# Kernel optimization log

Measured on AMD Instinct MI355X. Metric: run time of the kernel, lower is better.

## Reference

```python
import jax, jax.numpy as jnp
import numpy as np

T, N, L = 512, 128, 256           # encoder steps, batch, decode steps
KV, VS = 128, 128                 # key_size, value_size
EMB, HID, VOC = 256, 512, 34


def _lstm_cell(x, h, c, W_ih, W_hh, b_ih, b_hh):
    # PyTorch LSTMCell gate order: i, f, g, o
    g = x @ W_ih.T + b_ih + h @ W_hh.T + b_hh
    i, f, gg, o = jnp.split(g, 4, axis=-1)
    c2 = jax.nn.sigmoid(f) * c + jax.nn.sigmoid(i) * jnp.tanh(gg)
    h2 = jax.nn.sigmoid(o) * jnp.tanh(c2)
    return h2, c2


def setup_inputs() -> dict:
    k = jax.random.key(0)
    ks = jax.random.split(k, 16)
    s = 0.05
    return {
        "key": jax.random.normal(ks[0], (T, N, KV), jnp.float32),
        "values": jax.random.normal(ks[1], (T, N, VS), jnp.float32),
        "lens": jax.random.randint(ks[2], (N,), 1, T + 1),
        "text": jax.random.randint(ks[3], (N, L), 0, VOC),
        "emb": jax.random.normal(ks[4], (VOC, EMB), jnp.float32) * s,
        "W_ih1": jax.random.normal(ks[5], (4 * HID, EMB + VS), jnp.float32) * s,
        "W_hh1": jax.random.normal(ks[6], (4 * HID, HID), jnp.float32) * s,
        "b_ih1": jnp.zeros((4 * HID,), jnp.float32),
        "b_hh1": jnp.zeros((4 * HID,), jnp.float32),
        "W_ih2": jax.random.normal(ks[7], (4 * KV, HID), jnp.float32) * s,
        "W_hh2": jax.random.normal(ks[8], (4 * KV, KV), jnp.float32) * s,
        "b_ih2": jnp.zeros((4 * KV,), jnp.float32),
        "b_hh2": jnp.zeros((4 * KV,), jnp.float32),
        "W_out": jax.random.normal(ks[9], (VOC, KV + VS), jnp.float32) * s,
        "b_out": jnp.zeros((VOC,), jnp.float32),
    }


def reference(key, values, lens, text, emb, W_ih1, W_hh1, b_ih1, b_hh1,
              W_ih2, W_hh2, b_ih2, b_hh2, W_out, b_out):
    # key/values: (T, N, 128); teacher-forced decode over L steps.
    pad_mask = jnp.arange(T)[None, :] >= lens[:, None]        # (N, T)
    embs = emb[text]                                          # (N, L, EMB)
    embs = jnp.transpose(embs, (1, 0, 2))                     # (L, N, EMB)

    def step(carry, e_t):
        h1, c1, h2, c2, ctx = carry
        x = jnp.concatenate([e_t, ctx], axis=-1)
        h1, c1 = _lstm_cell(x, h1, c1, W_ih1, W_hh1, b_ih1, b_hh1)
        h2, c2 = _lstm_cell(h1, h2, c2, W_ih2, W_hh2, b_ih2, b_hh2)
        # masked bmm attention: energy (N, T)
        energy = jnp.einsum('tnk,nk->nt', key, h2)
        energy = jnp.where(pad_mask, -1e9, energy)
        attn = jax.nn.softmax(energy, axis=1)
        ctx = jnp.einsum('nt,tnv->nv', attn, values)
        pred = jnp.concatenate([h2, ctx], axis=-1) @ W_out.T + b_out
        return (h1, c1, h2, c2, ctx), pred

    init = (jnp.zeros((N, HID)), jnp.zeros((N, HID)),
            jnp.zeros((N, KV)), jnp.zeros((N, KV)),
            jnp.zeros((N, VS)))
    _, preds = jax.lax.scan(step, init, embs)                 # (L, N, VOC)
    return jnp.transpose(preds, (1, 0, 2))                    # (N, L, VOC)
```

## Files before the change

kernel.cpp:

```cpp
#include <hip/hip_runtime.h>
#include <hip/hip_cooperative_groups.h>
#include <math.h>

#define LDEC 256
#define VOCD 34
#define SPIN_MAX 2000000u
#define XSTR 660

typedef __attribute__((ext_vector_type(8))) short bf16x8;
typedef __attribute__((ext_vector_type(8))) unsigned short u16x8;
typedef __attribute__((ext_vector_type(4))) float f32x4;

#define OFF_W1H  0u
#define OFF_W1L  2621440u
#define OFF_W2H  5242880u
#define OFF_W2L  5898240u
#define OFF_EG   6553600u
#define OFF_B2   6832128u
#define OFF_WOT  6834176u
#define OFF_H1P  6868992u
#define OFF_H2P  7393280u
#define OFF_CTXP 7524352u
#define OFF_C1   7589888u
#define OFF_C2   7852032u
#define OFF_FLG  7917568u
#define OFF_KB   7966720u
#define OFF_VB   24743936u
#define WS_NEED  41521152u

__device__ __forceinline__ float sigf(float x) { return 1.0f / (1.0f + expf(-x)); }
__device__ __forceinline__ unsigned short f2b(float x) {
  unsigned int u = __float_as_uint(x);
  unsigned int r = (u + 0x7FFFu + ((u >> 16) & 1u)) >> 16;
  return (unsigned short)r;
}
__device__ __forceinline__ float b2f(unsigned short h) {
  return __uint_as_float(((unsigned int)h) << 16);
}
__device__ __forceinline__ unsigned packf(float x) {
  unsigned short hi = f2b(x);
  unsigned short lo = f2b(x - b2f(hi));
  return ((unsigned)hi << 16) | (unsigned)lo;
}
__device__ __forceinline__ float unpackf(unsigned p) {
  return b2f((unsigned short)(p >> 16)) + b2f((unsigned short)(p & 0xffffu));
}
__device__ __forceinline__ unsigned aload(const unsigned* p) {
  return __hip_atomic_load((unsigned*)p, __ATOMIC_RELAXED, __HIP_MEMORY_SCOPE_SYSTEM);
}
__device__ __forceinline__ void astore(unsigned* p, unsigned v) {
  __hip_atomic_store(p, v, __ATOMIC_RELAXED, __HIP_MEMORY_SCOPE_SYSTEM);
}
__device__ __forceinline__ void unpack8(const unsigned* p, bf16x8& xh, bf16x8& xl) {
#pragma unroll
  for (int j = 0; j < 8; j++) {
    unsigned v = p[j];
    xh[j] = (short)(v >> 16);
    xl[j] = (short)(v & 0xffffu);
  }
}

__global__ __launch_bounds__(256) void pack_w1(const float* __restrict__ Wih1,
                                               const float* __restrict__ Whh1,
                                               unsigned short* __restrict__ W1H,
                                               unsigned short* __restrict__ W1L) {
  int idx = blockIdx.x * 256 + threadIdx.x;
  int m = idx / 640, k = idx % 640;
  int u = m >> 2, q = m & 3;
  int g = q * 512 + u;
  float v = (k < 128) ? Wih1[g * 384 + 256 + k] : Whh1[g * 512 + (k - 128)];
  unsigned short hi = f2b(v);
  W1H[idx] = hi;
  W1L[idx] = f2b(v - b2f(hi));
}

__global__ __launch_bounds__(256) void pack_w2(const float* __restrict__ Wih2,
                                               const float* __restrict__ Whh2,
                                               unsigned short* __restrict__ W2H,
                                               unsigned short* __restrict__ W2L) {
  int idx = blockIdx.x * 256 + threadIdx.x;
  int m = idx / 640, k = idx % 640;
  int u = m >> 2, q = m & 3;
  int g = q * 128 + u;
  float v = (k < 512) ? Wih2[g * 512 + k] : Whh2[g * 128 + (k - 512)];
  unsigned short hi = f2b(v);
  W2H[idx] = hi;
  W2L[idx] = f2b(v - b2f(hi));
}

__global__ __launch_bounds__(256) void pack_eg(const float* __restrict__ emb,
                                               const float* __restrict__ Wih1,
                                               const float* __restrict__ bih1,
                                               const float* __restrict__ bhh1,
                                               float* __restrict__ EG) {
  int idx = blockIdx.x * 256 + threadIdx.x;
  int v = idx >> 11, m = idx & 2047;
  int u = m >> 2, q = m & 3;
  int g = q * 512 + u;
  float acc = bih1[g] + bhh1[g];
  const float* e = emb + v * 256;
  const float* w = Wih1 + g * 384;
  for (int k = 0; k < 256; k++) acc += e[k] * w[k];
  EG[idx] = acc;
}

__global__ __launch_bounds__(256) void pack_misc(const float* __restrict__ Wout,
                                                 const float* __restrict__ bih2,
                                                 const float* __restrict__ bhh2,
                                                 float* __restrict__ WoT,
                                                 float* __restrict__ B2) {
  int idx = blockIdx.x * 256 + threadIdx.x;
  if (idx < 8704) {
    int k = idx / 34, v = idx % 34;
    WoT[idx] = Wout[v * 256 + k];
  } else if (idx < 9216) {
    int m = idx - 8704;
    int u = m >> 2, q = m & 3;
    int g = q * 128 + u;
    B2[m] = bih2[g] + bhh2[g];
  }
}

__global__ __launch_bounds__(256) void pack_kv(const float* __restrict__ key,
                                               const float* __restrict__ values,
                                               unsigned short* __restrict__ KB,
                                               unsigned short* __restrict__ VB) {
  size_t idx = (size_t)blockIdx.x * 256 + threadIdx.x;
  KB[idx] = f2b(key[idx]);
  VB[idx] = f2b(values[idx]);
}

__device__ __forceinline__ void stage_h1(int gang, int tid, int rbuf,
                                         unsigned* xshA, const unsigned* __restrict__ H1P) {
  int kcol = tid & 15, nl = (tid >> 4) & 15, rep = tid >> 8;
  int n = gang * 16 + nl;
  const unsigned* h1p = H1P + rbuf * 65536 + n * 512;
#pragma unroll
  for (int j = 0; j < 10; j++) {
    int k = rep * 160 + j * 16 + kcol;
    if (k >= 128) xshA[nl * XSTR + k] = aload(h1p + (k - 128));
  }
}
__device__ __forceinline__ void stage_ctx(int gang, int tid,
                                          unsigned* xshA, const unsigned* __restrict__ CTXP) {
  int kcol = tid & 15, nl = (tid >> 4) & 15, rep = tid >> 8;
  int n = gang * 16 + nl;
  if (rep == 0) {
#pragma unroll
    for (int j = 0; j < 8; j++) {
      int k = j * 16 + kcol;
      xshA[nl * XSTR + k] = aload(CTXP + n * 128 + k);
    }
  }
}

__device__ __forceinline__ void A_compute(
    int gang, int gidx, int tid, int t, int wp,
    const unsigned* __restrict__ xshA, float* bred,
    const unsigned short* __restrict__ W1H, const unsigned short* __restrict__ W1L,
    const float* __restrict__ EG, const int* __restrict__ text,
    unsigned* __restrict__ H1P, float* __restrict__ C1)
{
  const int wid = tid >> 6, lane = tid & 63;
  const int l15 = lane & 15, lg = lane >> 4;
  const int gr = wid >> 2, gwid = wid & 3;
  const int kb0 = gwid * 160;
  const int mt = (gidx & 7) * 16 + (gidx >> 3) * 4 + gr;

  {
    const unsigned short* whp = W1H + (size_t)(mt * 16 + l15) * 640 + kb0 + lg * 8;
    const unsigned short* wlp = W1L + (size_t)(mt * 16 + l15) * 640 + kb0 + lg * 8;
    const unsigned* xrow = xshA + l15 * XSTR + kb0 + lg * 8;
    f32x4 a0 = {0.0f, 0.0f, 0.0f, 0.0f};
    f32x4 a1 = {0.0f, 0.0f, 0.0f, 0.0f};
    f32x4 a2 = {0.0f, 0.0f, 0.0f, 0.0f};
#pragma unroll
    for (int ks = 0; ks < 5; ks++) {
      unsigned parr[8];
      *(uint4*)parr       = *(const uint4*)(xrow + ks * 32);
      *(uint4*)(parr + 4) = *(const uint4*)(xrow + ks * 32 + 4);
      bf16x8 xh_, xl_;
      unpack8(parr, xh_, xl_);
      bf16x8 wh_ = *(const bf16x8*)(whp + ks * 32);
      bf16x8 wl_ = *(const bf16x8*)(wlp + ks * 32);
      a0 = __builtin_amdgcn_mfma_f32_16x16x32_bf16(wh_, xh_, a0, 0, 0, 0);
      a1 = __builtin_amdgcn_mfma_f32_16x16x32_bf16(wl_, xh_, a1, 0, 0, 0);
      a2 = __builtin_amdgcn_mfma_f32_16x16x32_bf16(wh_, xl_, a2, 0, 0, 0);
    }
    f32x4 acc = a0 + a1;
    acc = acc + a2;
#pragma unroll
    for (int q = 0; q < 4; q++) bred[gr * 1024 + q * 256 + gwid * 64 + lane] = acc[q];
  }
  __syncthreads();

  if (gwid == 0) {
    const float* br = bred + gr * 1024;
    int n = gang * 16 + l15;
    int tok = text[n * LDEC + t];
    f32x4 egv = *(const f32x4*)(EG + (size_t)tok * 2048 + mt * 16 + lg * 4);
    float g0 = br[lane]       + br[64 + lane]  + br[128 + lane] + br[192 + lane] + egv[0];
    float g1 = br[256 + lane] + br[320 + lane] + br[384 + lane] + br[448 + lane] + egv[1];
    float g2 = br[512 + lane] + br[576 + lane] + br[640 + lane] + br[704 + lane] + egv[2];
    float g3 = br[768 + lane] + br[832 + lane] + br[896 + lane] + br[960 + lane] + egv[3];
    float ig = sigf(g0), fg = sigf(g1), gg = tanhf(g2), og = sigf(g3);
    int u = mt * 4 + lg;
    float c = fg * C1[u * 128 + n] + ig * gg;
    float h = og * tanhf(c);
    C1[u * 128 + n] = c;
    astore(H1P + wp * 65536 + n * 512 + u, packf(h));
  }
  __syncthreads();
}

__device__ __forceinline__ void dev_phaseB(
    int gang, int gidx, int tid, int rp, int wp, float* bred,
    const unsigned short* __restrict__ W2H, const unsigned short* __restrict__ W2L,
    const float* __restrict__ B2,
    const unsigned* __restrict__ H1P, unsigned* __restrict__ H2P,
    float* __restrict__ C2)
{
  const int wid = tid >> 6, lane = tid & 63;
  const int l15 = lane & 15, lg = lane >> 4;
  const int mtB = (gidx & 7) * 4 + (gidx >> 3);
  if (tid < 256) {
    const int kb0 = wid * 160;
    int n = gang * 16 + l15;
    const unsigned* x1 = H1P + wp * 65536 + n * 512;
    const unsigned* x2 = H2P + rp * 16384 + n * 128;
    const unsigned short* whp = W2H + (size_t)(mtB * 16 + l15) * 640 + kb0 + lg * 8;
    const unsigned short* wlp = W2L + (size_t)(mtB * 16 + l15) * 640 + kb0 + lg * 8;
    f32x4 a0 = {0.0f, 0.0f, 0.0f, 0.0f};
    f32x4 a1 = {0.0f, 0.0f, 0.0f, 0.0f};
    f32x4 a2 = {0.0f, 0.0f, 0.0f, 0.0f};
#pragma unroll
    for (int ks = 0; ks < 5; ks++) {
      int kb = kb0 + ks * 32;
      unsigned parr[8];
      const unsigned* src = (kb < 512) ? (x1 + kb + lg * 8) : (x2 + (kb - 512) + lg * 8);
#pragma unroll
      for (int j = 0; j < 8; j++) parr[j] = aload(src + j);
      bf16x8 xh_, xl_;
      unpack8(parr, xh_, xl_);
      bf16x8 wh_ = *(const bf16x8*)(whp + ks * 32);
      bf16x8 wl_ = *(const bf16x8*)(wlp + ks * 32);
      a0 = __builtin_amdgcn_mfma_f32_16x16x32_bf16(wh_, xh_, a0, 0, 0, 0);
      a1 = __builtin_amdgcn_mfma_f32_16x16x32_bf16(wl_, xh_, a1, 0, 0, 0);
      a2 = __builtin_amdgcn_mfma_f32_16x16x32_bf16(wh_, xl_, a2, 0, 0, 0);
    }
    f32x4 acc = a0 + a1;
    acc = acc + a2;
#pragma unroll
    for (int q = 0; q < 4; q++) bred[q * 256 + wid * 64 + lane] = acc[q];
  }
  __syncthreads();
  if (tid < 64) {
    f32x4 b2v = *(const f32x4*)(B2 + mtB * 16 + lg * 4);
    float g0 = bred[lane]       + bred[64 + lane]  + bred[128 + lane] + bred[192 + lane] + b2v[0];
    float g1 = bred[256 + lane] + bred[320 + lane] + bred[384 + lane] + bred[448 + lane] + b2v[1];
    float g2 = bred[512 + lane] + bred[576 + lane] + bred[640 + lane] + bred[704 + lane] + b2v[2];
    float g3 = bred[768 + lane] + bred[832 + lane] + bred[896 + lane] + bred[960 + lane] + b2v[3];
    int n = gang * 16 + l15;
    int u = mtB * 4 + lg;
    float c = sigf(g1) * C2[u * 128 + n] + sigf(g0) * tanhf(g2);
    float h = sigf(g3) * tanhf(c);
    C2[u * 128 + n] = c;
    astore(H2P + wp * 16384 + n * 128 + u, packf(h));
  }
  __syncthreads();
}

template <int BF16KV>
__device__ __forceinline__ void dev_phaseC(
    int n, int tid, int len, int t, int wp,
    float* cred, float* es, float* h2s, float* ctxs, float* pr, float* sred,
    const float* __restrict__ key, const float* __restrict__ values,
    const unsigned short* __restrict__ KB, const unsigned short* __restrict__ VB,
    const unsigned* __restrict__ H2P, const float* __restrict__ WoT,
    const float* __restrict__ bout, unsigned* __restrict__ CTXP,
    float* __restrict__ out, unsigned* sCslot, unsigned tv)
{
  const int wid = tid >> 6, lane = tid & 63;
  if (tid < 128) h2s[tid] = unpackf(aload(H2P + wp * 16384 + n * 128 + tid));
  __syncthreads();
  float ls = 0.0f;
  if (tid < len) {
    float acc = 0.0f;
    if (BF16KV) {
      const u16x8* kr = (const u16x8*)(KB + ((size_t)tid * 128 + n) * 128);
#pragma unroll 4
      for (int k = 0; k < 16; k++) {
        u16x8 kv = kr[k];
#pragma unroll
        for (int j = 0; j < 8; j++) acc += b2f(kv[j]) * h2s[k * 8 + j];
      }
    } else {
      const float4* kr = (const float4*)(key + ((size_t)tid * 128 + n) * 128);
#pragma unroll 8
      for (int k = 0; k < 32; k++) {
        float4 kv = kr[k];
        acc += kv.x * h2s[4 * k] + kv.y * h2s[4 * k + 1] + kv.z * h2s[4 * k + 2] + kv.w * h2s[4 * k + 3];
      }
    }
    float p = expf(acc - 20.0f);
    es[tid] = p;
    ls = p;
  }
  ls += __shfl_xor(ls, 32); ls += __shfl_xor(ls, 16); ls += __shfl_xor(ls, 8);
  ls += __shfl_xor(ls, 4);  ls += __shfl_xor(ls, 2);  ls += __shfl_xor(ls, 1);
  if (lane == 0) sred[wid] = ls;
  __syncthreads();
  float S = 0.0f;
#pragma unroll
  for (int w = 0; w < 16; w++) S += sred[w];
  {
    int v4 = (tid & 31) * 4, tp = tid >> 5;
    float ax = 0.0f, ay = 0.0f, az = 0.0f, aw = 0.0f;
    if (BF16KV) {
#pragma unroll 2
      for (int tt = tp; tt < len; tt += 32) {
        float p = es[tt];
        const unsigned* w = (const unsigned*)(VB + ((size_t)tt * 128 + n) * 128 + v4);
        unsigned w0 = w[0], w1 = w[1];
        ax += p * b2f((unsigned short)(w0 & 0xffffu));
        ay += p * b2f((unsigned short)(w0 >> 16));
        az += p * b2f((unsigned short)(w1 & 0xffffu));
        aw += p * b2f((unsigned short)(w1 >> 16));
      }
    } else {
#pragma unroll 2
      for (int tt = tp; tt < len; tt += 32) {
        float p = es[tt];
        const float4 vv = *(const float4*)(values + ((size_t)tt * 128 + n) * 128 + v4);
        ax += p * vv.x; ay += p * vv.y; az += p * vv.z; aw += p * vv.w;
      }
    }
    float4 a4 = {ax, ay, az, aw};
    *(float4*)&cred[tp * 132 + v4] = a4;
  }
  __syncthreads();
  if (tid < 128) {
    float s4 = 0.0f;
#pragma unroll 8
    for (int tp2 = 0; tp2 < 32; tp2++) s4 += cred[tp2 * 132 + tid];
    float cv = s4 / S;
    ctxs[tid] = cv;
    astore(CTXP + n * 128 + tid, packf(cv));
  }
  __syncthreads();
  if (sCslot && tid == 0) astore(sCslot, tv);
  if (tid < 68) {
    int vv = tid % 34, part = tid / 34;
    const float* src = part ? ctxs : h2s;
    const float* wcol = WoT + (part ? 128 * 34 : 0);
    float a = 0.0f;
#pragma unroll 8
    for (int k2 = 0; k2 < 128; k2++) a += src[k2] * wcol[k2 * 34 + vv];
    pr[tid] = a;
  }
  __syncthreads();
  if (tid < 34) {
    out[(size_t)n * (LDEC * VOCD) + t * VOCD + tid] = bout[tid] + pr[tid] + pr[34 + tid];
  }
  __syncthreads();
}

__global__ void __launch_bounds__(1024, 1) kA(
    const unsigned short* __restrict__ W1H, const unsigned short* __restrict__ W1L,
    const float* __restrict__ EG, const int* __restrict__ text,
    const unsigned* __restrict__ CTXP, unsigned* __restrict__ H1P,
    float* __restrict__ C1, int t, int rp, int wp)
{
  __shared__ unsigned xshA[16 * XSTR];
  __shared__ float bred[4096];
  const int gang = blockIdx.x >> 5, gidx = blockIdx.x & 31;
  stage_h1(gang, threadIdx.x, rp, xshA, H1P);
  stage_ctx(gang, threadIdx.x, xshA, CTXP);
  __syncthreads();
  A_compute(gang, gidx, threadIdx.x, t, wp, xshA, bred, W1H, W1L, EG, text, H1P, C1);
}
__global__ void __launch_bounds__(256) kB(
    const unsigned short* __restrict__ W2H, const unsigned short* __restrict__ W2L,
    const float* __restrict__ B2, const unsigned* __restrict__ H1P,
    unsigned* __restrict__ H2P, float* __restrict__ C2, int rp, int wp)
{
  __shared__ float bred[1024];
  dev_phaseB(blockIdx.x >> 5, blockIdx.x & 31, threadIdx.x, rp, wp, bred,
             W2H, W2L, B2, H1P, H2P, C2);
}
template <int BF16KV>
__global__ void __launch_bounds__(1024, 1) kC(
    const float* __restrict__ key, const float* __restrict__ values,
    const unsigned short* __restrict__ KB, const unsigned short* __restrict__ VB,
    const int* __restrict__ lens, const unsigned* __restrict__ H2P,
    const float* __restrict__ WoT, const float* __restrict__ bout,
    unsigned* __restrict__ CTXP, float* __restrict__ out, int t, int wp)
{
  __shared__ float cred[4224];
  __shared__ float es[512];
  __shared__ float h2s[128];
  __shared__ float ctxs[128];
  __shared__ float pr[68];
  __shared__ float sred[16];
  int n = blockIdx.x;
  dev_phaseC<BF16KV>(n, threadIdx.x, lens[n], t, wp, cred, es, h2s, ctxs, pr, sred,
                     key, values, KB, VB, H2P, WoT, bout, CTXP, out,
                     (unsigned*)0, 0u);
}

template <int BF16KV>
__global__ void __launch_bounds__(1024, 1) decoder_coop(
    const float* __restrict__ key, const float* __restrict__ values,
    const unsigned short* __restrict__ KB, const unsigned short* __restrict__ VB,
    const int* __restrict__ lens, const int* __restrict__ text,
    const float* __restrict__ EG, const float* __restrict__ B2,
    const float* __restrict__ WoT, const float* __restrict__ bout,
    const unsigned short* __restrict__ W1H, const unsigned short* __restrict__ W1L,
    const unsigned short* __restrict__ W2H, const unsigned short* __restrict__ W2L,
    unsigned* __restrict__ CTXP, unsigned* __restrict__ H1P,
    unsigned* __restrict__ H2P, float* __restrict__ C1, float* __restrict__ C2,
    unsigned* __restrict__ FLG, float* __restrict__ out)
{
  __shared__ unsigned xshA[16 * XSTR];
  __shared__ float bred[4096];
  __shared__ float cred[4224];
  __shared__ float es[512];
  __shared__ float h2s[128];
  __shared__ float ctxs[128];
  __shared__ float pr[68];
  __shared__ float sred[16];
  __shared__ unsigned deadsh;

  const int bid = blockIdx.x, tid = threadIdx.x;
  const int gang = bid >> 5, gidx = bid & 31;
  unsigned* sA = FLG + gang * 512;
  unsigned* sB = FLG + 4096 + gang * 512;
  unsigned* sC = FLG + 8192 + gang * 256;
  const int cn = gang * 16 + gidx;
  const int clen = (gidx < 16) ? lens[cn] : 0;

  unsigned budget = SPIN_MAX;
  if (tid == 0) deadsh = 0u;

  stage_h1(gang, tid, 1, xshA, H1P);
  __syncthreads();

  for (int t = 0; t < LDEC; t++) {
    const int wp = t & 1, rp = (t + 1) & 1;
    const unsigned tv = (unsigned)(t + 1);

    stage_ctx(gang, tid, xshA, CTXP);
    __syncthreads();
    A_compute(gang, gidx, tid, t, wp, xshA, bred, W1H, W1L, EG, text, H1P, C1);
    if (tid == 0) astore(sA + gidx * 16, tv);
    if (tid < 32) {
      unsigned* s = sA + tid * 16;
      while (aload(s) < tv) {
        if (--budget == 0) { deadsh = 1u; break; }
      }
    }
    __syncthreads();

    dev_phaseB(gang, gidx, tid, rp, wp, bred, W2H, W2L, B2, H1P, H2P, C2);
    if (tid == 0) astore(sB + gidx * 16, tv);

    stage_h1(gang, tid, wp, xshA, H1P);

    if (gidx < 16) {
      if (tid < 32) {
        unsigned* s = sB + tid * 16;
        while (aload(s) < tv) {
          if (--budget == 0) { deadsh = 1u; break; }
        }
      }
      __syncthreads();
      dev_phaseC<BF16KV>(cn, tid, clen, t, wp, cred, es, h2s, ctxs, pr, sred,
                         key, values, KB, VB, H2P, WoT, bout, CTXP, out,
                         sC + gidx * 16, tv);
    }
    if (tid < 16) {
      unsigned* s = sC + tid * 16;
      while (aload(s) < tv) {
        if (--budget == 0) { deadsh = 1u; break; }
      }
    }
    __syncthreads();
  }

  if (tid == 0 && deadsh) out[0] = 7.0e6f;
}

extern "C" void kernel_launch(void* const* d_in, const int* in_sizes, int n_in,
                              void* d_out, int out_size, void* d_ws, size_t ws_size,
                              hipStream_t stream) {
  const float* key    = (const float*)d_in[0];
  const float* values = (const float*)d_in[1];
  const int*   lens   = (const int*)d_in[2];
  const int*   text   = (const int*)d_in[3];
  const float* emb    = (const float*)d_in[4];
  const float* Wih1   = (const float*)d_in[5];
  const float* Whh1   = (const float*)d_in[6];
  const float* bih1   = (const float*)d_in[7];
  const float* bhh1   = (const float*)d_in[8];
  const float* Wih2   = (const float*)d_in[9];
  const float* Whh2   = (const float*)d_in[10];
  const float* bih2   = (const float*)d_in[11];
  const float* bhh2   = (const float*)d_in[12];
  const float* Wout   = (const float*)d_in[13];
  const float* bout   = (const float*)d_in[14];

  char* ws = (char*)d_ws;
  unsigned short* W1H = (unsigned short*)(ws + OFF_W1H);
  unsigned short* W1L = (unsigned short*)(ws + OFF_W1L);
  unsigned short* W2H = (unsigned short*)(ws + OFF_W2H);
  unsigned short* W2L = (unsigned short*)(ws + OFF_W2L);
  float* EG   = (float*)(ws + OFF_EG);
  float* B2   = (float*)(ws + OFF_B2);
  float* WoT  = (float*)(ws + OFF_WOT);
  unsigned* H1P  = (unsigned*)(ws + OFF_H1P);
  unsigned* H2P  = (unsigned*)(ws + OFF_H2P);
  unsigned* CTXP = (unsigned*)(ws + OFF_CTXP);
  float* C1   = (float*)(ws + OFF_C1);
  float* C2   = (float*)(ws + OFF_C2);
  unsigned* FLG = (unsigned*)(ws + OFF_FLG);
  unsigned short* KB = (unsigned short*)(ws + OFF_KB);
  unsigned short* VB = (unsigned short*)(ws + OFF_VB);
  float* out  = (float*)d_out;

  const bool use16 = (ws_size >= (size_t)WS_NEED);

  hipMemsetAsync(CTXP, 0, 65536, stream);
  hipMemsetAsync((char*)H1P + 262144, 0, 262144, stream);
  hipMemsetAsync((char*)H2P + 65536, 0, 65536, stream);
  hipMemsetAsync(C1,  0, 262144, stream);
  hipMemsetAsync(C2,  0, 65536, stream);
  hipMemsetAsync(FLG, 0, 49152, stream);

  pack_w1  <<<5120, 256, 0, stream>>>(Wih1, Whh1, W1H, W1L);
  pack_w2  <<<1280, 256, 0, stream>>>(Wih2, Whh2, W2H, W2L);
  pack_eg  <<<272,  256, 0, stream>>>(emb, Wih1, bih1, bhh1, EG);
  pack_misc<<<36,   256, 0, stream>>>(Wout, bih2, bhh2, WoT, B2);
  if (use16) pack_kv<<<32768, 256, 0, stream>>>(key, values, KB, VB);

  const void* coop_fn = use16 ? (const void*)decoder_coop<1>
                              : (const void*)decoder_coop<0>;

  int maxBlk = 0;
  hipError_t qerr = hipOccupancyMaxActiveBlocksPerMultiprocessor(
      &maxBlk, coop_fn, 1024, 0);
  bool coop_ok = (qerr == hipSuccess && maxBlk >= 1);

  if (coop_ok) {
    void* args[] = {
      (void*)&key, (void*)&values, (void*)&KB, (void*)&VB,
      (void*)&lens, (void*)&text,
      (void*)&EG, (void*)&B2, (void*)&WoT, (void*)&bout,
      (void*)&W1H, (void*)&W1L, (void*)&W2H, (void*)&W2L,
      (void*)&CTXP, (void*)&H1P, (void*)&H2P, (void*)&C1, (void*)&C2,
      (void*)&FLG, (void*)&out
    };
    hipError_t err = hipLaunchCooperativeKernel(coop_fn, dim3(256), dim3(1024),
                                                args, 0, stream);
    if (err == hipSuccess) return;
  }

  for (int t = 0; t < LDEC; t++) {
    const int wp = t & 1, rp = (t + 1) & 1;
    kA<<<256, 1024, 0, stream>>>(W1H, W1L, EG, text, CTXP, H1P, C1, t, rp, wp);
    kB<<<256, 256,  0, stream>>>(W2H, W2L, B2, H1P, H2P, C2, rp, wp);
    if (use16)
      kC<1><<<128, 1024, 0, stream>>>(key, values, KB, VB, lens, H2P, WoT, bout,
                                      CTXP, out, t, wp);
    else
      kC<0><<<128, 1024, 0, stream>>>(key, values, KB, VB, lens, H2P, WoT, bout,
                                      CTXP, out, t, wp);
  }
}
```

Measured before the change: 7.853 ms.

## Split LSTM1 gate GEMM so hidden-state part overlaps attention phase

The layer-1 gate matmul is split into a pre part covering the h1 columns and a post part covering the ctx columns, which depend on the attention output. The h1 contribution for step t+1 is computed right after h1 is staged, before waiting on phase C. Only the ctx-dependent k-slices stay on the critical path after the ctx flag. This adds an extra __syncthreads and keeps accumulators live across the step, which raises register pressure.

```diff
diff --git a/kernel.cpp b/kernel.cpp
--- a/kernel.cpp
+++ b/kernel.cpp
@@ -154,12 +154,11 @@
   }
 }
 
-__device__ __forceinline__ void A_compute(
-    int gang, int gidx, int tid, int t, int wp,
-    const unsigned* __restrict__ xshA, float* bred,
+__device__ __forceinline__ void A_pre(
+    int gidx, int tid,
+    const unsigned* __restrict__ xshA,
     const unsigned short* __restrict__ W1H, const unsigned short* __restrict__ W1L,
-    const float* __restrict__ EG, const int* __restrict__ text,
-    unsigned* __restrict__ H1P, float* __restrict__ C1)
+    f32x4& p0, f32x4& p1, f32x4& p2)
 {
   const int wid = tid >> 6, lane = tid & 63;
   const int l15 = lane & 15, lg = lane >> 4;
@@ -167,15 +166,49 @@
   const int kb0 = gwid * 160;
   const int mt = (gidx & 7) * 16 + (gidx >> 3) * 4 + gr;
 
-  {
-    const unsigned short* whp = W1H + (size_t)(mt * 16 + l15) * 640 + kb0 + lg * 8;
-    const unsigned short* wlp = W1L + (size_t)(mt * 16 + l15) * 640 + kb0 + lg * 8;
-    const unsigned* xrow = xshA + l15 * XSTR + kb0 + lg * 8;
-    f32x4 a0 = {0.0f, 0.0f, 0.0f, 0.0f};
-    f32x4 a1 = {0.0f, 0.0f, 0.0f, 0.0f};
-    f32x4 a2 = {0.0f, 0.0f, 0.0f, 0.0f};
-#pragma unroll
-    for (int ks = 0; ks < 5; ks++) {
+  const unsigned short* whp = W1H + (size_t)(mt * 16 + l15) * 640 + kb0 + lg * 8;
+  const unsigned short* wlp = W1L + (size_t)(mt * 16 + l15) * 640 + kb0 + lg * 8;
+  const unsigned* xrow = xshA + l15 * XSTR + kb0 + lg * 8;
+  f32x4 a0 = {0.0f, 0.0f, 0.0f, 0.0f};
+  f32x4 a1 = {0.0f, 0.0f, 0.0f, 0.0f};
+  f32x4 a2 = {0.0f, 0.0f, 0.0f, 0.0f};
+  const int ks0 = (gwid == 0) ? 4 : 0;
+#pragma unroll
+  for (int ks = 0; ks < 5; ks++) {
+    if (ks < ks0) continue;
+    unsigned parr[8];
+    *(uint4*)parr       = *(const uint4*)(xrow + ks * 32);
+    *(uint4*)(parr + 4) = *(const uint4*)(xrow + ks * 32 + 4);
+    bf16x8 xh_, xl_;
+    unpack8(parr, xh_, xl_);
+    bf16x8 wh_ = *(const bf16x8*)(whp + ks * 32);
+    bf16x8 wl_ = *(const bf16x8*)(wlp + ks * 32);
+    a0 = __builtin_amdgcn_mfma_f32_16x16x32_bf16(wh_, xh_, a0, 0, 0, 0);
+    a1 = __builtin_amdgcn_mfma_f32_16x16x32_bf16(wl_, xh_, a1, 0, 0, 0);
+    a2 = __builtin_amdgcn_mfma_f32_16x16x32_bf16(wh_, xl_, a2, 0, 0, 0);
+  }
+  p0 = a0; p1 = a1; p2 = a2;
+}
+
+__device__ __forceinline__ void A_post(
+    int gang, int gidx, int tid, int t, int wp,
+    const unsigned* __restrict__ xshA, float* bred,
+    const unsigned short* __restrict__ W1H, const unsigned short* __restrict__ W1L,
+    const float* __restrict__ EG, const int* __restrict__ text,
+    unsigned* __restrict__ H1P, float* __restrict__ C1,
+    f32x4 p0, f32x4 p1, f32x4 p2)
+{
+  const int wid = tid >> 6, lane = tid & 63;
+  const int l15 = lane & 15, lg = lane >> 4;
+  const int gr = wid >> 2, gwid = wid & 3;
+  const int mt = (gidx & 7) * 16 + (gidx >> 3) * 4 + gr;
+
+  if (gwid == 0) {
+    const unsigned short* whp = W1H + (size_t)(mt * 16 + l15) * 640 + lg * 8;
+    const unsigned short* wlp = W1L + (size_t)(mt * 16 + l15) * 640 + lg * 8;
+    const unsigned* xrow = xshA + l15 * XSTR + lg * 8;
+#pragma unroll
+    for (int ks = 0; ks < 4; ks++) {
       unsigned parr[8];
       *(uint4*)parr       = *(const uint4*)(xrow + ks * 32);
       *(uint4*)(parr + 4) = *(const uint4*)(xrow + ks * 32 + 4);
@@ -183,15 +216,15 @@
       unpack8(parr, xh_, xl_);
       bf16x8 wh_ = *(const bf16x8*)(whp + ks * 32);
       bf16x8 wl_ = *(const bf16x8*)(wlp + ks * 32);
-      a0 = __builtin_amdgcn_mfma_f32_16x16x32_bf16(wh_, xh_, a0, 0, 0, 0);
-      a1 = __builtin_amdgcn_mfma_f32_16x16x32_bf16(wl_, xh_, a1, 0, 0, 0);
-      a2 = __builtin_amdgcn_mfma_f32_16x16x32_bf16(wh_, xl_, a2, 0, 0, 0);
-    }
-    f32x4 acc = a0 + a1;
-    acc = acc + a2;
-#pragma unroll
-    for (int q = 0; q < 4; q++) bred[gr * 1024 + q * 256 + gwid * 64 + lane] = acc[q];
-  }
+      p0 = __builtin_amdgcn_mfma_f32_16x16x32_bf16(wh_, xh_, p0, 0, 0, 0);
+      p1 = __builtin_amdgcn_mfma_f32_16x16x32_bf16(wl_, xh_, p1, 0, 0, 0);
+      p2 = __builtin_amdgcn_mfma_f32_16x16x32_bf16(wh_, xl_, p2, 0, 0, 0);
+    }
+  }
+  f32x4 acc = p0 + p1;
+  acc = acc + p2;
+#pragma unroll
+  for (int q = 0; q < 4; q++) bred[gr * 1024 + q * 256 + gwid * 64 + lane] = acc[q];
   __syncthreads();
 
   if (gwid == 0) {
@@ -211,6 +244,18 @@
     astore(H1P + wp * 65536 + n * 512 + u, packf(h));
   }
   __syncthreads();
+}
+
+__device__ __forceinline__ void A_compute(
+    int gang, int gidx, int tid, int t, int wp,
+    const unsigned* __restrict__ xshA, float* bred,
+    const unsigned short* __restrict__ W1H, const unsigned short* __restrict__ W1L,
+    const float* __restrict__ EG, const int* __restrict__ text,
+    unsigned* __restrict__ H1P, float* __restrict__ C1)
+{
+  f32x4 p0, p1, p2;
+  A_pre(gidx, tid, xshA, W1H, W1L, p0, p1, p2);
+  A_post(gang, gidx, tid, t, wp, xshA, bred, W1H, W1L, EG, text, H1P, C1, p0, p1, p2);
 }
 
 __device__ __forceinline__ void dev_phaseB(
@@ -444,6 +489,8 @@
 
   stage_h1(gang, tid, 1, xshA, H1P);
   __syncthreads();
+  f32x4 p0, p1, p2;
+  A_pre(gidx, tid, xshA, W1H, W1L, p0, p1, p2);
 
   for (int t = 0; t < LDEC; t++) {
     const int wp = t & 1, rp = (t + 1) & 1;
@@ -451,7 +498,8 @@
 
     stage_ctx(gang, tid, xshA, CTXP);
     __syncthreads();
-    A_compute(gang, gidx, tid, t, wp, xshA, bred, W1H, W1L, EG, text, H1P, C1);
+    A_post(gang, gidx, tid, t, wp, xshA, bred, W1H, W1L, EG, text, H1P, C1,
+           p0, p1, p2);
     if (tid == 0) astore(sA + gidx * 16, tv);
     if (tid < 32) {
       unsigned* s = sA + tid * 16;
@@ -465,6 +513,8 @@
     if (tid == 0) astore(sB + gidx * 16, tv);
 
     stage_h1(gang, tid, wp, xshA, H1P);
+    __syncthreads();
+    if (t < LDEC - 1) A_pre(gidx, tid, xshA, W1H, W1L, p0, p1, p2);
 
     if (gidx < 16) {
       if (tid < 32) {
```

Measured after the change: 7.883 ms. No clear change (+0.4%).
